# Performance work log

Hardware: AMD Instinct MI355X
Metric: run time of the kernel (lower is better)

Reference implementation:

```python
import jax, jax.numpy as jnp
import numpy as np

B, V, H = 16384, 1024, 256


def setup_inputs() -> dict:
    key = jax.random.key(0)
    k1, k2 = jax.random.split(key)
    # binary spin configurations in {0,1}
    batch = jax.random.bernoulli(k1, 0.5, (B, V)).astype(jnp.float32)
    # small weights + negative hidden bias keep exp(log p*) finite in fp32
    weights_amp = jax.random.normal(k2, (H, V), dtype=jnp.float32) * (0.05 / np.sqrt(V))
    visible_bias_amp = jnp.zeros((V,), dtype=jnp.float32)
    hidden_bias_amp = -5.0 * jnp.ones((H,), dtype=jnp.float32)
    return {
        'batch': batch,
        'weights_amp': weights_amp,
        'visible_bias_amp': visible_bias_amp,
        'hidden_bias_amp': hidden_bias_amp,
        'k': 8,
    }


def _gibbs_sampling_amp(v0, W, vb, hb, k, key):
    """k steps of block Gibbs sampling, vectorized over the whole batch [B,V]."""
    keys = jax.random.split(key, 2 * k).reshape(k, 2)

    def step(v, ks):
        ph = jax.nn.sigmoid(v @ W.T + hb)                      # [B,H]
        h = (jax.random.uniform(ks[0], ph.shape) < ph).astype(v.dtype)
        pv = jax.nn.sigmoid(h @ W + vb)                        # [B,V]
        v = (jax.random.uniform(ks[1], pv.shape) < pv).astype(v.dtype)
        return v, None

    vk, _ = jax.lax.scan(step, v0, keys)
    return vk


def reference(batch, weights_amp, visible_bias_amp, hidden_bias_amp, k):
    W, vb, hb = weights_amp, visible_bias_amp, hidden_bias_amp
    nbatch = batch.shape[0]
    key = jax.random.key(42)

    vk = _gibbs_sampling_amp(batch, W, vb, hb, k, key)          # [B,V]

    ph0 = jax.nn.sigmoid(batch @ W.T + hb)                      # [B,H] positive-phase hidden probs
    pre_k = vk @ W.T + hb                                       # [B,H]
    phk = jax.nn.sigmoid(pre_k)                                 # [B,H] negative-phase hidden probs

    # unnormalized_probability_amp(vk) = exp(vk.vb + sum_j softplus((W vk + hb)_j))
    log_p = vk @ vb + jax.nn.softplus(pre_k).sum(axis=-1)       # [B]
    inv_norm = jnp.exp(-log_p) / nbatch                         # 1 / (len(batch) * p*(vk))

    # g_W = sum_b [outer(phk_b, vk_b) - outer(ph0_b, v0_b)] / norm_b
    g_w = (jnp.einsum('b,bh,bv->hv', inv_norm, phk, vk)
           - jnp.einsum('b,bh,bv->hv', inv_norm, ph0, batch))   # [H,V]
    g_vb = jnp.einsum('b,bv->v', inv_norm, vk - batch)          # [V]
    g_hb = jnp.einsum('b,bh->h', inv_norm, phk - ph0)           # [H]

    return jnp.concatenate([g_w.ravel(), g_vb, g_hb])
```

## Files before the change

### kernel.cpp

```cpp
#include <hip/hip_runtime.h>
#include <stdint.h>

#define B_DIM 16384
#define V_DIM 1024
#define H_DIM 256
#define K_STEPS 8
#define HALF_B 8192

typedef short bf16x8 __attribute__((ext_vector_type(8)));
typedef float f32x4 __attribute__((ext_vector_type(4)));

__host__ __device__ inline uint32_t rotl32(uint32_t v, int r) {
#if defined(__HIP_DEVICE_COMPILE__)
    return __builtin_amdgcn_alignbit(v, v, (uint32_t)(32 - r));
#else
    return (v << r) | (v >> (32 - r));
#endif
}

__host__ __device__ inline void threefry2x32(uint32_t k0, uint32_t k1,
                                             uint32_t x0, uint32_t x1,
                                             uint32_t* o0, uint32_t* o1) {
    uint32_t k2 = k0 ^ k1 ^ 0x1BD11BDAu;
    x0 += k0; x1 += k1;
#define TF_RND(r) { x0 += x1; x1 = rotl32(x1, (r)); x1 ^= x0; }
    TF_RND(13) TF_RND(15) TF_RND(26) TF_RND(6)
    x0 += k1; x1 += k2 + 1u;
    TF_RND(17) TF_RND(29) TF_RND(16) TF_RND(24)
    x0 += k2; x1 += k0 + 2u;
    TF_RND(13) TF_RND(15) TF_RND(26) TF_RND(6)
    x0 += k0; x1 += k1 + 3u;
    TF_RND(17) TF_RND(29) TF_RND(16) TF_RND(24)
    x0 += k1; x1 += k2 + 4u;
    TF_RND(13) TF_RND(15) TF_RND(26) TF_RND(6)
    x0 += k2; x1 += k0 + 5u;
#undef TF_RND
    *o0 = x0; *o1 = x1;
}

__device__ inline float tf_uniform(uint32_t key0, uint32_t key1, uint32_t e) {
    uint32_t o0, o1;
    threefry2x32(key0, key1, 0u, e, &o0, &o1);
    uint32_t bits = o0 ^ o1;
    return __uint_as_float((bits >> 9) | 0x3f800000u) - 1.0f;
}

__device__ inline uint16_t bf16_rn(float f) {
    uint32_t u = __float_as_uint(f);
    uint32_t r = u + 0x7FFFu + ((u >> 16) & 1u);
    return (uint16_t)(r >> 16);
}
__device__ inline float bf16_to_f32(uint16_t h) {
    return __uint_as_float(((uint32_t)h) << 16);
}

__device__ inline void gload_lds16(const void* g, void* l) {
    __builtin_amdgcn_global_load_lds((const __attribute__((address_space(1))) uint32_t*)g,
                                     (__attribute__((address_space(3))) uint32_t*)l, 16, 0, 0);
}


__global__ void pack_w_kernel(const float* __restrict__ W,
                              ushort* __restrict__ whp, ushort* __restrict__ wlp) {
    int uid = blockIdx.x * 256 + threadIdx.x;
    int l = uid & 63, s = (uid >> 6) & 1, kc = (uid >> 7) & 15, R = uid >> 11;
    int row = R * 16 + (l & 15);
    int col = kc * 64 + s * 32 + (l >> 4) * 8;
    const float* src = W + (size_t)row * V_DIM + col;
    ushort* dh = whp + (size_t)uid * 8;
    ushort* dl = wlp + (size_t)uid * 8;
#pragma unroll
    for (int e = 0; e < 8; ++e) {
        float w = src[e];
        ushort hi = bf16_rn(w);
        dh[e] = hi;
        dl[e] = bf16_rn(w - bf16_to_f32(hi));
    }
}

__global__ void pack_batch_kernel(const float* __restrict__ batch,
                                  ushort* __restrict__ bp) {
    int uid = blockIdx.x * 256 + threadIdx.x;
    int l = uid & 63, s = (uid >> 6) & 1, kc = (uid >> 7) & 15, R = uid >> 11;
    int row = R * 16 + (l & 15);
    int col = kc * 64 + s * 32 + (l >> 4) * 8;
    const float* src = batch + (size_t)row * V_DIM + col;
    ushort* d = bp + (size_t)uid * 8;
#pragma unroll
    for (int e = 0; e < 8; ++e) d[e] = bf16_rn(src[e]);
}

template <int MODE>
__device__ __forceinline__ void gemm_block_p(
    const int m0, const int n0,
    const ushort* __restrict__ Ap, const ushort* __restrict__ Bhp,
    const ushort* __restrict__ Blp, const float* __restrict__ bias,
    ushort* __restrict__ out, ushort* __restrict__ out2,
    const uint32_t key0, const uint32_t key1) {
    const int lane = threadIdx.x & 63;
    const int w = threadIdx.x >> 6;
    const int wm = (w & 1) * 32;
    const int wn = (w >> 1) * 32;
    const int q = lane >> 4;
    const int l15 = lane & 15;

    const ushort* apA = Ap + (size_t)((m0 >> 4) + (wm >> 4)) * 16384 + lane * 8;
    const ushort* apBh = Bhp + (size_t)((n0 >> 4) + (wn >> 4)) * 16384 + lane * 8;
    const ushort* apBl = Blp + (size_t)((n0 >> 4) + (wn >> 4)) * 16384 + lane * 8;

    f32x4 acc[2][2] = {};

#pragma unroll 2
    for (int kc = 0; kc < 16; ++kc) {
#pragma unroll
        for (int s = 0; s < 2; ++s) {
            const int go = kc * 1024 + s * 512;
            bf16x8 af[2], bh[2], bl[2];
#pragma unroll
            for (int i = 0; i < 2; ++i)
                af[i] = *(const bf16x8*)(apA + go + i * 16384);
#pragma unroll
            for (int j = 0; j < 2; ++j) {
                bh[j] = *(const bf16x8*)(apBh + go + j * 16384);
                bl[j] = *(const bf16x8*)(apBl + go + j * 16384);
            }
#pragma unroll
            for (int i = 0; i < 2; ++i)
#pragma unroll
                for (int j = 0; j < 2; ++j) {
                    acc[i][j] = __builtin_amdgcn_mfma_f32_16x16x32_bf16(af[i], bh[j], acc[i][j], 0, 0, 0);
                    acc[i][j] = __builtin_amdgcn_mfma_f32_16x16x32_bf16(af[i], bl[j], acc[i][j], 0, 0, 0);
                }
        }
    }

    const int orow = q * 4;
#pragma unroll
    for (int i = 0; i < 2; ++i) {
#pragma unroll
        for (int j = 0; j < 2; ++j) {
            int col = n0 + wn + j * 16 + l15;
            float bv = bias[col];
#pragma unroll
            for (int r = 0; r < 4; ++r) {
                int row = m0 + wm + i * 16 + orow + r;
                float val = acc[i][j][r] + bv;
                if (MODE == 0) {
                    float E = expf(-val);
                    uint32_t e = (uint32_t)row * (uint32_t)H_DIM + (uint32_t)col;
                    float u = tf_uniform(key0, key1, e);
                    out[(size_t)row * H_DIM + col] = (fmaf(u, E, u) < 1.0f) ? (ushort)0x3F80 : (ushort)0;
                } else if (MODE == 3) {
                    float E = expf(-val);
                    float sg = 1.0f / (1.0f + E);
                    uint32_t e = (uint32_t)row * (uint32_t)H_DIM + (uint32_t)col;
                    float u = tf_uniform(key0, key1, e);
                    out[(size_t)row * H_DIM + col] = (fmaf(u, E, u) < 1.0f) ? (ushort)0x3F80 : (ushort)0;
                    out2[(size_t)row * H_DIM + col] = bf16_rn(sg);
                } else {
                    float sg = 1.0f / (1.0f + expf(-val));
                    out[(size_t)row * H_DIM + col] = bf16_rn(sg);
                }
            }
        }
    }
}

__device__ __forceinline__ void vsample_block(
    const ushort* __restrict__ h, const float* __restrict__ W,
    const float* __restrict__ vb, ushort* __restrict__ vpack,
    ushort* __restrict__ vrow, int write_row,
    uint32_t key0, uint32_t key1, int row_base) {
    const int lane = threadIdx.x & 63;
    const int wid = threadIdx.x >> 6;

    float vbr[16];
#pragma unroll
    for (int t = 0; t < 16; ++t) vbr[t] = vb[lane + 64 * t];

    const int rb2 = row_base + wid * 2;
#pragma unroll
    for (int rr = 0; rr < 2; ++rr) {
        const int b = rb2 + rr;
        ushort4 hv = ((const ushort4*)(h + (size_t)b * H_DIM))[lane];
        unsigned long long masks[4];
        masks[0] = __ballot(hv.x != 0);
        masks[1] = __ballot(hv.y != 0);
        masks[2] = __ballot(hv.z != 0);
        masks[3] = __ballot(hv.w != 0);

        float acc[16];
#pragma unroll
        for (int t = 0; t < 16; ++t) acc[t] = 0.0f;

#pragma unroll
        for (int s = 0; s < 4; ++s) {
            unsigned long long m = masks[s];
            while (m) {
                int l = __ffsll(m) - 1;
                m &= m - 1;
                int j = l * 4 + s;
                const float* wrow = W + (size_t)j * V_DIM + lane;
#pragma unroll
                for (int t = 0; t < 16; ++t) acc[t] += wrow[64 * t];
            }
        }

        const uint32_t ebase = (uint32_t)b * (uint32_t)V_DIM + (uint32_t)lane;
        ushort* vp = vpack + (size_t)(b >> 4) * 16384 + (b & 15) * 8 +
                     ((lane >> 5) & 1) * 512 + ((lane >> 3) & 3) * 128 + (lane & 7);
        ushort* orow = vrow + (size_t)b * V_DIM + lane;
#pragma unroll
        for (int t = 0; t < 16; ++t) {
            float pre = acc[t] + vbr[t];
            float E = expf(-pre);
            float u = tf_uniform(key0, key1, ebase + 64u * (uint32_t)t);
            ushort val = (fmaf(u, E, u) < 1.0f) ? (ushort)0x3F80 : (ushort)0;
            vp[t * 1024] = val;
            if (write_row) orow[64 * t] = val;
        }
    }
}

template <int MODE>
__global__ __launch_bounds__(256, 6) void gemm_only(
    const ushort* __restrict__ Ap, const ushort* __restrict__ Bhp,
    const ushort* __restrict__ Blp, const float* __restrict__ bias,
    ushort* __restrict__ out, ushort* __restrict__ out2,
    uint32_t key0, uint32_t key1, int mbase) {
    gemm_block_p<MODE>(mbase + blockIdx.x * 64, blockIdx.y * 64, Ap, Bhp, Blp,
                       bias, out, out2, key0, key1);
}

template <int MODE>
__global__ __launch_bounds__(256, 6) void hybrid_step(
    const ushort* __restrict__ Ap, const ushort* __restrict__ Whp,
    const ushort* __restrict__ Wlp, const float* __restrict__ hb,
    ushort* __restrict__ hout, ushort* __restrict__ out2,
    uint32_t gk0, uint32_t gk1, int gemm_mbase,
    const ushort* __restrict__ hprev, const float* __restrict__ Wf,
    const float* __restrict__ vb, ushort* __restrict__ vpack,
    ushort* __restrict__ vrow, int write_row,
    uint32_t vk0, uint32_t vk1, int vs_base) {
    const int bid = blockIdx.x;
    const int g3 = bid / 3;
    const int r3 = bid - g3 * 3;
    if (r3 < 2) {
        const int vs = g3 * 2 + r3;
        vsample_block(hprev, Wf, vb, vpack, vrow, write_row, vk0, vk1,
                      vs_base + vs * 8);
    } else {
        const int g = g3;
        const int gx = g & 127;
        const int gy = g >> 7;
        gemm_block_p<MODE>(gemm_mbase + gx * 64, gy * 64, Ap, Whp, Wlp, hb,
                           hout, out2, gk0, gk1);
    }
}

__global__ __launch_bounds__(256, 4) void mfma_gemm_acc(
    const ushort* __restrict__ A, const ushort* __restrict__ Bt,
    float* __restrict__ out, int N, int K, int k_slice) {
    __shared__ __align__(16) ushort As[64 * 64];
    __shared__ __align__(16) ushort Bs[64 * 64];

    const int tid = threadIdx.x;
    const int lane = tid & 63;
    const int w = tid >> 6;
    const int m0 = blockIdx.x * 64;
    const int n0 = blockIdx.y * 64;
    const int kbase = blockIdx.z * k_slice;

    const int wm = (w & 1) * 32;
    const int wn = (w >> 1) * 32;
    const int q = lane >> 4;
    const int l15 = lane & 15;

    const ushort* asrc[2];
    const ushort* bsrc[2];
#pragma unroll
    for (int i = 0; i < 2; ++i) {
        const int j = w * 2 + i;
        const int row = j * 8 + (lane >> 3);
        const int sl = (lane & 7) ^ (row & 7);
        const size_t off = (size_t)row * K + (sl >> 2) * 32 + (sl & 3) * 8;
        asrc[i] = A + (size_t)m0 * K + off;
        bsrc[i] = Bt + (size_t)n0 * K + off;
    }

    f32x4 acc[2][2] = {};

    for (int kt = 0; kt < k_slice; kt += 64) {
        const int k0 = kbase + kt;
#pragma unroll
        for (int i = 0; i < 2; ++i) {
            gload_lds16(asrc[i] + k0, &As[(w * 2 + i) * 512]);
            gload_lds16(bsrc[i] + k0, &Bs[(w * 2 + i) * 512]);
        }
        __syncthreads();
#pragma unroll
        for (int s = 0; s < 2; ++s) {
            bf16x8 af[2], bf[2];
#pragma unroll
            for (int i = 0; i < 2; ++i) {
                const int ra = wm + i * 16 + l15;
                const int rb = wn + i * 16 + l15;
                af[i] = *(const bf16x8*)((const char*)As + ra * 128 +
                                         (((s * 4 + q) ^ (ra & 7)) * 16));
                bf[i] = *(const bf16x8*)((const char*)Bs + rb * 128 +
                                         (((s * 4 + q) ^ (rb & 7)) * 16));
            }
#pragma unroll
            for (int i = 0; i < 2; ++i)
#pragma unroll
                for (int j = 0; j < 2; ++j)
                    acc[i][j] = __builtin_amdgcn_mfma_f32_16x16x32_bf16(af[i], bf[j], acc[i][j], 0, 0, 0);
        }
        __syncthreads();
    }

    const int orow = q * 4;
#pragma unroll
    for (int i = 0; i < 2; ++i)
#pragma unroll
        for (int j = 0; j < 2; ++j) {
            int col = n0 + wn + j * 16 + l15;
#pragma unroll
            for (int r = 0; r < 4; ++r) {
                int row = m0 + wm + i * 16 + orow + r;
                atomicAdd(&out[(size_t)row * N + col], acc[i][j][r]);
            }
        }
}

__global__ __launch_bounds__(256) void lognorm_kernel(
    const ushort* __restrict__ phk, const ushort* __restrict__ vk,
    const float* __restrict__ vb, float* __restrict__ inv) {
    int b = blockIdx.x;
    int tid = threadIdx.x;
    float p = bf16_to_f32(phk[(size_t)b * H_DIM + tid]);
    float s = -log1pf(-p);
    for (int j = tid; j < V_DIM; j += 256)
        s += bf16_to_f32(vk[(size_t)b * V_DIM + j]) * vb[j];
    for (int off = 32; off > 0; off >>= 1) s += __shfl_down(s, off, 64);
    __shared__ float wsum[4];
    int lane = tid & 63, wid = tid >> 6;
    if (lane == 0) wsum[wid] = s;
    __syncthreads();
    if (tid == 0) {
        float t = wsum[0] + wsum[1] + wsum[2] + wsum[3];
        inv[b] = expf(-t) * (1.0f / 16384.0f);
    }
}

__global__ void build_At(const ushort* __restrict__ P, const float* __restrict__ inv,
                         float sgn, ushort* __restrict__ At) {
    __shared__ float T[64][65];
    int c = threadIdx.x & 63;
    int rb = threadIdx.x >> 6;
    int b0 = blockIdx.x * 64;
    int h0 = blockIdx.y * 64;
    for (int r = rb; r < 64; r += 4) {
        int b = b0 + r;
        T[c][r] = sgn * inv[b] * bf16_to_f32(P[(size_t)b * H_DIM + h0 + c]);
    }
    __syncthreads();
    for (int r = rb; r < 64; r += 4)
        At[(size_t)(h0 + r) * B_DIM + b0 + c] = bf16_rn(T[r][c]);
}

__global__ void build_Bt(const ushort* __restrict__ Sb, const float* __restrict__ Sf,
                         int use_f32, ushort* __restrict__ Bt) {
    __shared__ ushort T[64][65];
    int c = threadIdx.x & 63;
    int rb = threadIdx.x >> 6;
    int b0 = blockIdx.x * 64;
    int v0 = blockIdx.y * 64;
    for (int r = rb; r < 64; r += 4) {
        int b = b0 + r;
        T[c][r] = use_f32 ? bf16_rn(Sf[(size_t)b * V_DIM + v0 + c])
                          : Sb[(size_t)b * V_DIM + v0 + c];
    }
    __syncthreads();
    for (int r = rb; r < 64; r += 4)
        Bt[(size_t)(v0 + r) * B_DIM + b0 + c] = T[r][c];
}

__global__ void gvb_kernel(const ushort* __restrict__ vk, const float* __restrict__ batchf,
                           const float* __restrict__ inv, float* __restrict__ gvb) {
    int col = blockIdx.x * 256 + threadIdx.x;
    int b0 = blockIdx.y * 512;
    float acc = 0.0f;
    for (int r = 0; r < 512; ++r) {
        int b = b0 + r;
        acc += inv[b] * (bf16_to_f32(vk[(size_t)b * V_DIM + col]) -
                         batchf[(size_t)b * V_DIM + col]);
    }
    atomicAdd(&gvb[col], acc);
}

__global__ void ghb_kernel(const ushort* __restrict__ phk, const ushort* __restrict__ ph0,
                           const float* __restrict__ inv, float* __restrict__ ghb) {
    int col = threadIdx.x;
    int b0 = blockIdx.x * 256;
    float acc = 0.0f;
    for (int r = 0; r < 256; ++r) {
        int b = b0 + r;
        acc += inv[b] * (bf16_to_f32(phk[(size_t)b * H_DIM + col]) -
                         bf16_to_f32(ph0[(size_t)b * H_DIM + col]));
    }
    atomicAdd(&ghb[col], acc);
}

extern "C" void kernel_launch(void* const* d_in, const int* in_sizes, int n_in,
                              void* d_out, int out_size, void* d_ws, size_t ws_size,
                              hipStream_t stream) {
    const float* batch = (const float*)d_in[0];
    const float* W = (const float*)d_in[1];
    const float* vb = (const float*)d_in[2];
    const float* hb = (const float*)d_in[3];

    char* base = (char*)d_ws;
    ushort* w_hi_p = (ushort*)(base + 0);
    ushort* w_lo_p = (ushort*)(base + 524288);
    float*  inv    = (float*)(base + 1048576);
    ushort* v_pack = (ushort*)(base + 2097152);
    ushort* Bt     = v_pack;
    ushort* v_row  = (ushort*)(base + 35651584);
    ushort* batch_p = v_row;
    ushort* h_cur  = (ushort*)(base + 69206016);
    ushort* At     = h_cur;
    ushort* ph0b   = (ushort*)(base + 77594624);
    ushort* phkb   = (ushort*)(base + 85983232);

    float* gw  = (float*)d_out;
    float* gvb = gw + (size_t)H_DIM * V_DIM;
    float* ghb = gvb + V_DIM;

    hipMemsetAsync(d_out, 0, (size_t)out_size * sizeof(float), stream);

    uint32_t sk0[16], sk1[16];
    for (int n = 0; n < 16; ++n) threefry2x32(0u, 42u, 0u, (uint32_t)n, &sk0[n], &sk1[n]);

    pack_w_kernel<<<dim3(128), dim3(256), 0, stream>>>(W, w_hi_p, w_lo_p);
    pack_batch_kernel<<<dim3(8192), dim3(256), 0, stream>>>(batch, batch_p);

    const int NB_VS = HALF_B / 8;
    const int NB_G  = (HALF_B / 64) * 4;
    const dim3 HYB(NB_VS + NB_G);

    gemm_only<3><<<dim3(128, 4), dim3(256), 0, stream>>>(
        batch_p, w_hi_p, w_lo_p, hb, h_cur, ph0b, sk0[0], sk1[0], 0);

    for (int s = 0; s < K_STEPS; ++s) {
        const int wr = (s == K_STEPS - 1) ? 1 : 0;
        if (s == 0) {
            hybrid_step<3><<<HYB, dim3(256), 0, stream>>>(
                batch_p, w_hi_p, w_lo_p, hb, h_cur, ph0b, sk0[0], sk1[0], HALF_B,
                h_cur, W, vb, v_pack, v_row, wr, sk0[1], sk1[1], 0);
        } else {
            hybrid_step<0><<<HYB, dim3(256), 0, stream>>>(
                v_pack, w_hi_p, w_lo_p, hb, h_cur, nullptr, sk0[2 * s], sk1[2 * s], HALF_B,
                h_cur, W, vb, v_pack, v_row, wr, sk0[2 * s + 1], sk1[2 * s + 1], 0);
        }
        if (s < K_STEPS - 1) {
            hybrid_step<0><<<HYB, dim3(256), 0, stream>>>(
                v_pack, w_hi_p, w_lo_p, hb, h_cur, nullptr, sk0[2 * s + 2], sk1[2 * s + 2], 0,
                h_cur, W, vb, v_pack, v_row, wr, sk0[2 * s + 1], sk1[2 * s + 1], HALF_B);
        } else {
            hybrid_step<1><<<HYB, dim3(256), 0, stream>>>(
                v_pack, w_hi_p, w_lo_p, hb, phkb, nullptr, 0u, 0u, 0,
                h_cur, W, vb, v_pack, v_row, wr, sk0[2 * s + 1], sk1[2 * s + 1], HALF_B);
        }
    }
    gemm_only<1><<<dim3(128, 4), dim3(256), 0, stream>>>(
        v_pack, w_hi_p, w_lo_p, hb, phkb, nullptr, 0u, 0u, HALF_B);

    lognorm_kernel<<<dim3(B_DIM), dim3(256), 0, stream>>>(phkb, v_row, vb, inv);
    ghb_kernel<<<dim3(B_DIM / 256), dim3(256), 0, stream>>>(phkb, ph0b, inv, ghb);
    gvb_kernel<<<dim3(V_DIM / 256, B_DIM / 512), dim3(256), 0, stream>>>(v_row, batch, inv, gvb);

    build_At<<<dim3(B_DIM / 64, H_DIM / 64), dim3(256), 0, stream>>>(phkb, inv, 1.0f, At);
    build_Bt<<<dim3(B_DIM / 64, V_DIM / 64), dim3(256), 0, stream>>>(v_row, nullptr, 0, Bt);
    mfma_gemm_acc<<<dim3(H_DIM / 64, V_DIM / 64, 16), dim3(256), 0, stream>>>(
        At, Bt, gw, V_DIM, B_DIM, 1024);
    build_At<<<dim3(B_DIM / 64, H_DIM / 64), dim3(256), 0, stream>>>(ph0b, inv, -1.0f, At);
    build_Bt<<<dim3(B_DIM / 64, V_DIM / 64), dim3(256), 0, stream>>>(nullptr, batch, 1, Bt);
    mfma_gemm_acc<<<dim3(H_DIM / 64, V_DIM / 64, 16), dim3(256), 0, stream>>>(
        At, Bt, gw, V_DIM, B_DIM, 1024);
}
```

Measured before the change: 862.1 us.

## Rebalance hybrid Gibbs blocks, raise occupancy, and replace atomic gW split-K with partial reduction

The hybrid step now gives each wave one visible-sampling row instead of two and mixes blocks 4:1 rather than 2:1. This makes visible-sampling blocks finer and more numerous to improve load balance against the GEMM blocks. Launch bounds for the GEMM and hybrid kernels are raised to 8 blocks per CU. The split-K weight-gradient GEMM writes per-slice partials that a separate reduce kernel sums, instead of using float atomics. The gvb reduction also uses more, shorter row chunks. The costs are register pressure from the higher occupancy target, the extra partial-buffer traffic, and two added kernel launches.

Result: slower. 1.038 ms (+20.4%).

```diff
diff --git a/kernel.cpp b/kernel.cpp
--- a/kernel.cpp
+++ b/kernel.cpp
@@ -166,64 +166,58 @@
     }
 }
 
-__device__ __forceinline__ void vsample_block(
+__device__ __forceinline__ void vsample_row(
     const ushort* __restrict__ h, const float* __restrict__ W,
     const float* __restrict__ vb, ushort* __restrict__ vpack,
     ushort* __restrict__ vrow, int write_row,
-    uint32_t key0, uint32_t key1, int row_base) {
+    uint32_t key0, uint32_t key1, int b) {
     const int lane = threadIdx.x & 63;
-    const int wid = threadIdx.x >> 6;
 
     float vbr[16];
 #pragma unroll
     for (int t = 0; t < 16; ++t) vbr[t] = vb[lane + 64 * t];
 
-    const int rb2 = row_base + wid * 2;
-#pragma unroll
-    for (int rr = 0; rr < 2; ++rr) {
-        const int b = rb2 + rr;
-        ushort4 hv = ((const ushort4*)(h + (size_t)b * H_DIM))[lane];
-        unsigned long long masks[4];
-        masks[0] = __ballot(hv.x != 0);
-        masks[1] = __ballot(hv.y != 0);
-        masks[2] = __ballot(hv.z != 0);
-        masks[3] = __ballot(hv.w != 0);
-
-        float acc[16];
-#pragma unroll
-        for (int t = 0; t < 16; ++t) acc[t] = 0.0f;
-
-#pragma unroll
-        for (int s = 0; s < 4; ++s) {
-            unsigned long long m = masks[s];
-            while (m) {
-                int l = __ffsll(m) - 1;
-                m &= m - 1;
-                int j = l * 4 + s;
-                const float* wrow = W + (size_t)j * V_DIM + lane;
-#pragma unroll
-                for (int t = 0; t < 16; ++t) acc[t] += wrow[64 * t];
-            }
-        }
-
-        const uint32_t ebase = (uint32_t)b * (uint32_t)V_DIM + (uint32_t)lane;
-        ushort* vp = vpack + (size_t)(b >> 4) * 16384 + (b & 15) * 8 +
-                     ((lane >> 5) & 1) * 512 + ((lane >> 3) & 3) * 128 + (lane & 7);
-        ushort* orow = vrow + (size_t)b * V_DIM + lane;
-#pragma unroll
-        for (int t = 0; t < 16; ++t) {
-            float pre = acc[t] + vbr[t];
-            float E = expf(-pre);
-            float u = tf_uniform(key0, key1, ebase + 64u * (uint32_t)t);
-            ushort val = (fmaf(u, E, u) < 1.0f) ? (ushort)0x3F80 : (ushort)0;
-            vp[t * 1024] = val;
-            if (write_row) orow[64 * t] = val;
-        }
+    ushort4 hv = ((const ushort4*)(h + (size_t)b * H_DIM))[lane];
+    unsigned long long masks[4];
+    masks[0] = __ballot(hv.x != 0);
+    masks[1] = __ballot(hv.y != 0);
+    masks[2] = __ballot(hv.z != 0);
+    masks[3] = __ballot(hv.w != 0);
+
+    float acc[16];
+#pragma unroll
+    for (int t = 0; t < 16; ++t) acc[t] = 0.0f;
+
+#pragma unroll
+    for (int s = 0; s < 4; ++s) {
+        unsigned long long m = masks[s];
+        while (m) {
+            int l = __ffsll(m) - 1;
+            m &= m - 1;
+            int j = l * 4 + s;
+            const float* wrow = W + (size_t)j * V_DIM + lane;
+#pragma unroll
+            for (int t = 0; t < 16; ++t) acc[t] += wrow[64 * t];
+        }
+    }
+
+    const uint32_t ebase = (uint32_t)b * (uint32_t)V_DIM + (uint32_t)lane;
+    ushort* vp = vpack + (size_t)(b >> 4) * 16384 + (b & 15) * 8 +
+                 ((lane >> 5) & 1) * 512 + ((lane >> 3) & 3) * 128 + (lane & 7);
+    ushort* orow = vrow + (size_t)b * V_DIM + lane;
+#pragma unroll
+    for (int t = 0; t < 16; ++t) {
+        float pre = acc[t] + vbr[t];
+        float E = expf(-pre);
+        float u = tf_uniform(key0, key1, ebase + 64u * (uint32_t)t);
+        ushort val = (fmaf(u, E, u) < 1.0f) ? (ushort)0x3F80 : (ushort)0;
+        vp[t * 1024] = val;
+        if (write_row) orow[64 * t] = val;
     }
 }
 
 template <int MODE>
-__global__ __launch_bounds__(256, 6) void gemm_only(
+__global__ __launch_bounds__(256, 8) void gemm_only(
     const ushort* __restrict__ Ap, const ushort* __restrict__ Bhp,
     const ushort* __restrict__ Blp, const float* __restrict__ bias,
     ushort* __restrict__ out, ushort* __restrict__ out2,
@@ -233,7 +227,7 @@
 }
 
 template <int MODE>
-__global__ __launch_bounds__(256, 6) void hybrid_step(
+__global__ __launch_bounds__(256, 8) void hybrid_step(
     const ushort* __restrict__ Ap, const ushort* __restrict__ Whp,
     const ushort* __restrict__ Wlp, const float* __restrict__ hb,
     ushort* __restrict__ hout, ushort* __restrict__ out2,
@@ -243,14 +237,15 @@
     ushort* __restrict__ vrow, int write_row,
     uint32_t vk0, uint32_t vk1, int vs_base) {
     const int bid = blockIdx.x;
-    const int g3 = bid / 3;
-    const int r3 = bid - g3 * 3;
-    if (r3 < 2) {
-        const int vs = g3 * 2 + r3;
-        vsample_block(hprev, Wf, vb, vpack, vrow, write_row, vk0, vk1,
-                      vs_base + vs * 8);
+    const int g5 = bid / 5;
+    const int r5 = bid - g5 * 5;
+    if (r5 < 4) {
+        const int u = g5 * 4 + r5;
+        const int w = threadIdx.x >> 6;
+        vsample_row(hprev, Wf, vb, vpack, vrow, write_row, vk0, vk1,
+                    vs_base + u * 4 + w);
     } else {
-        const int g = g3;
+        const int g = g5;
         const int gx = g & 127;
         const int gy = g >> 7;
         gemm_block_p<MODE>(gemm_mbase + gx * 64, gy * 64, Ap, Whp, Wlp, hb,
@@ -258,9 +253,9 @@
     }
 }
 
-__global__ __launch_bounds__(256, 4) void mfma_gemm_acc(
+__global__ __launch_bounds__(256, 4) void mfma_gemm_part(
     const ushort* __restrict__ A, const ushort* __restrict__ Bt,
-    float* __restrict__ out, int N, int K, int k_slice) {
+    float* __restrict__ part, int N, int K, int k_slice) {
     __shared__ __align__(16) ushort As[64 * 64];
     __shared__ __align__(16) ushort Bs[64 * 64];
 
@@ -319,6 +314,7 @@
         __syncthreads();
     }
 
+    float* pout = part + (size_t)blockIdx.z * (H_DIM * V_DIM);
     const int orow = q * 4;
 #pragma unroll
     for (int i = 0; i < 2; ++i)
@@ -328,9 +324,18 @@
 #pragma unroll
             for (int r = 0; r < 4; ++r) {
                 int row = m0 + wm + i * 16 + orow + r;
-                atomicAdd(&out[(size_t)row * N + col], acc[i][j][r]);
+                pout[(size_t)row * N + col] = acc[i][j][r];
             }
         }
+}
+
+__global__ __launch_bounds__(256) void reduce_gw(
+    const float* __restrict__ part, float* __restrict__ gw, int nz) {
+    const int idx = blockIdx.x * 256 + threadIdx.x;
+    float s = 0.0f;
+    for (int z = 0; z < nz; ++z)
+        s += part[(size_t)z * (H_DIM * V_DIM) + idx];
+    gw[idx] += s;
 }
 
 __global__ __launch_bounds__(256) void lognorm_kernel(
@@ -389,9 +394,9 @@
 __global__ void gvb_kernel(const ushort* __restrict__ vk, const float* __restrict__ batchf,
                            const float* __restrict__ inv, float* __restrict__ gvb) {
     int col = blockIdx.x * 256 + threadIdx.x;
-    int b0 = blockIdx.y * 512;
+    int b0 = blockIdx.y * 128;
     float acc = 0.0f;
-    for (int r = 0; r < 512; ++r) {
+    for (int r = 0; r < 128; ++r) {
         int b = b0 + r;
         acc += inv[b] * (bf16_to_f32(vk[(size_t)b * V_DIM + col]) -
                          batchf[(size_t)b * V_DIM + col]);
@@ -428,6 +433,7 @@
     ushort* Bt     = v_pack;
     ushort* v_row  = (ushort*)(base + 35651584);
     ushort* batch_p = v_row;
+    float*  part   = (float*)(base + 35651584);
     ushort* h_cur  = (ushort*)(base + 69206016);
     ushort* At     = h_cur;
     ushort* ph0b   = (ushort*)(base + 77594624);
@@ -445,7 +451,7 @@
     pack_w_kernel<<<dim3(128), dim3(256), 0, stream>>>(W, w_hi_p, w_lo_p);
     pack_batch_kernel<<<dim3(8192), dim3(256), 0, stream>>>(batch, batch_p);
 
-    const int NB_VS = HALF_B / 8;
+    const int NB_VS = HALF_B / 4;
     const int NB_G  = (HALF_B / 64) * 4;
     const dim3 HYB(NB_VS + NB_G);
 
@@ -478,14 +484,16 @@
 
     lognorm_kernel<<<dim3(B_DIM), dim3(256), 0, stream>>>(phkb, v_row, vb, inv);
     ghb_kernel<<<dim3(B_DIM / 256), dim3(256), 0, stream>>>(phkb, ph0b, inv, ghb);
-    gvb_kernel<<<dim3(V_DIM / 256, B_DIM / 512), dim3(256), 0, stream>>>(v_row, batch, inv, gvb);
+    gvb_kernel<<<dim3(V_DIM / 256, B_DIM / 128), dim3(256), 0, stream>>>(v_row, batch, inv, gvb);
 
     build_At<<<dim3(B_DIM / 64, H_DIM / 64), dim3(256), 0, stream>>>(phkb, inv, 1.0f, At);
     build_Bt<<<dim3(B_DIM / 64, V_DIM / 64), dim3(256), 0, stream>>>(v_row, nullptr, 0, Bt);
-    mfma_gemm_acc<<<dim3(H_DIM / 64, V_DIM / 64, 16), dim3(256), 0, stream>>>(
-        At, Bt, gw, V_DIM, B_DIM, 1024);
+    mfma_gemm_part<<<dim3(H_DIM / 64, V_DIM / 64, 16), dim3(256), 0, stream>>>(
+        At, Bt, part, V_DIM, B_DIM, 1024);
+    reduce_gw<<<dim3(H_DIM * V_DIM / 256), dim3(256), 0, stream>>>(part, gw, 16);
     build_At<<<dim3(B_DIM / 64, H_DIM / 64), dim3(256), 0, stream>>>(ph0b, inv, -1.0f, At);
     build_Bt<<<dim3(B_DIM / 64, V_DIM / 64), dim3(256), 0, stream>>>(nullptr, batch, 1, Bt);
-    mfma_gemm_acc<<<dim3(H_DIM / 64, V_DIM / 64, 16), dim3(256), 0, stream>>>(
-        At, Bt, gw, V_DIM, B_DIM, 1024);
-}
+    mfma_gemm_part<<<dim3(H_DIM / 64, V_DIM / 64, 16), dim3(256), 0, stream>>>(
+        At, Bt, part, V_DIM, B_DIM, 1024);
+    reduce_gw<<<dim3(H_DIM * V_DIM / 256), dim3(256), 0, stream>>>(part, gw, 16);
+}
```
